# Performance work log

Measured on AMD Instinct MI355X. Metric: run time of the kernel, lower is better.

Reference implementation:

```python
import jax, jax.numpy as jnp
import numpy as np

B, T = 64, 256
IN, HID, OUT = 512, 1024, 256
NUM_DOMAINS = 20

def setup_inputs() -> dict:
    key = jax.random.key(0)
    k1, k2, k3, k4 = jax.random.split(key, 4)
    x = jax.random.normal(k1, (B, T, IN), dtype=jnp.float32)
    hetero_info = jax.random.randint(k2, (B, 2), 0, NUM_DOMAINS, dtype=jnp.int64)
    # embedding tables init N(0, 0.02) as in the torch module
    fc1_table = 0.02 * jax.random.normal(k3, (NUM_DOMAINS, IN * HID + HID), dtype=jnp.float32)
    fc2_table = 0.02 * jax.random.normal(k4, (NUM_DOMAINS, HID * OUT + OUT), dtype=jnp.float32)
    return {"x": x, "hetero_info": hetero_info, "fc1_table": fc1_table, "fc2_table": fc2_table}

def reference(x, hetero_info, fc1_table, fc2_table):
    domain_id = hetero_info[:, 0].astype(jnp.int32)
    Bn = domain_id.shape[0]
    fc1_param = fc1_table[domain_id]                     # (B, IN*HID + HID)
    w1 = fc1_param[:, : IN * HID].reshape(Bn, IN, HID)   # (B, IN, HID)
    b1 = fc1_param[:, IN * HID:].reshape(Bn, 1, HID)
    fc2_param = fc2_table[domain_id]                     # (B, HID*OUT + OUT)
    w2 = fc2_param[:, : HID * OUT].reshape(Bn, HID, OUT) # (B, HID, OUT)
    b2 = fc2_param[:, HID * OUT:].reshape(Bn, 1, OUT)
    h = jnp.einsum('bti,bih->bth', x, w1) + b1
    h = jax.nn.gelu(h, approximate=False)  # torch nn.GELU default = exact erf
    out = jnp.einsum('bth,bho->bto', h, w2) + b2
    return out
```

## Files before the change

kernel.cpp:

```cpp
#include <hip/hip_runtime.h>
#include <math.h>

#define B_  64
#define T_  256
#define IN_ 512
#define HID_ 1024
#define OUT_ 256
#define NDOM 20

typedef __bf16 bf16_t;
typedef __bf16 bf16x8 __attribute__((ext_vector_type(8)));
typedef __bf16 bf16x4 __attribute__((ext_vector_type(4)));
typedef float  f32x4  __attribute__((ext_vector_type(4)));

__device__ __forceinline__ unsigned f2bf_bits(float f) {
    unsigned u = __builtin_bit_cast(unsigned, f);
    return (u + 0x7FFFu + ((u >> 16) & 1u)) >> 16;
}
__device__ __forceinline__ unsigned pack_bf16x2(float x, float y) {
    return f2bf_bits(x) | (f2bf_bits(y) << 16);
}

__device__ __forceinline__ void gl_lds16(const void* g, void* l) {
    __builtin_amdgcn_global_load_lds(
        (const __attribute__((address_space(1))) unsigned*)g,
        (__attribute__((address_space(3))) unsigned*)l,
        16, 0, 0);
}

__device__ __forceinline__ float gelu_fast(float v) {
    const float t = v * 0.70710678118654752f;
    const float a = __builtin_fabsf(t);
    const float k = __builtin_amdgcn_rcpf(__builtin_fmaf(0.3275911f, a, 1.0f));
    float p = __builtin_fmaf(1.061405429f, k, -1.453152027f);
    p = __builtin_fmaf(p, k, 1.421413741f);
    p = __builtin_fmaf(p, k, -0.284496736f);
    p = __builtin_fmaf(p, k, 0.254829592f);
    p = p * k;
    const float e  = __expf(-a * a);
    const float er = __builtin_fmaf(-p, e, 1.0f);
    const float erf_t = __builtin_copysignf(er, t);
    return 0.5f * v * (1.0f + erf_t);
}

__global__ __launch_bounds__(256) void prep_all(
    const float* __restrict__ X,  bf16_t* __restrict__ Xbf,
    const float* __restrict__ T1, const float* __restrict__ T2,
    bf16_t* __restrict__ W1t, bf16_t* __restrict__ W2t,
    float* __restrict__ b1, float* __restrict__ b2)
{
    const int tid = threadIdx.x;
    int blk = blockIdx.x;

    if (blk < 2048) {
        #pragma unroll
        for (int r = 0; r < 4; ++r) {
            const size_t idx = (size_t)blk * 1024 + r * 256 + tid;
            float4 v = ((const float4*)X)[idx];
            uint2 p;
            p.x = pack_bf16x2(v.x, v.y);
            p.y = pack_bf16x2(v.z, v.w);
            ((uint2*)Xbf)[idx] = p;
        }
        return;
    }

    const float* table; bf16_t* Wt; float* Bias;
    int K, N, d, n0, k0;
    if (blk < 4608) {
        blk -= 2048;
        d = blk >> 7; const int rem = blk & 127;
        k0 = (rem >> 4) * 64; n0 = (rem & 15) * 64;
        K = 512; N = 1024; table = T1; Wt = W1t; Bias = b1;
    } else {
        blk -= 4608;
        d = blk >> 6; const int rem = blk & 63;
        k0 = (rem >> 2) * 64; n0 = (rem & 3) * 64;
        K = 1024; N = 256; table = T2; Wt = W2t; Bias = b2;
    }
    const float* W = table + (size_t)d * ((size_t)K * N + N);

    __shared__ float t[64][65];

    #pragma unroll
    for (int r = 0; r < 4; ++r) {
        const int kl = (tid >> 4) + r * 16;
        const int nl = (tid & 15) * 4;
        float4 v = *(const float4*)(W + (size_t)(k0 + kl) * N + n0 + nl);
        t[kl][nl + 0] = v.x; t[kl][nl + 1] = v.y;
        t[kl][nl + 2] = v.z; t[kl][nl + 3] = v.w;
    }
    __syncthreads();

    bf16_t* Wtd = Wt + (size_t)d * K * N;
    #pragma unroll
    for (int r = 0; r < 4; ++r) {
        const int nl = (tid >> 4) + r * 16;
        const int k4 = (tid & 15) * 4;
        uint2 p;
        p.x = pack_bf16x2(t[k4 + 0][nl], t[k4 + 1][nl]);
        p.y = pack_bf16x2(t[k4 + 2][nl], t[k4 + 3][nl]);
        *(uint2*)(Wtd + (size_t)(n0 + nl) * K + k0 + k4) = p;
    }

    if (k0 == 0 && tid < 64)
        Bias[(size_t)d * N + n0 + tid] = W[(size_t)K * N + n0 + tid];
}

#define CT_STRIDE 136
__global__ __launch_bounds__(256) void fc1_gemm(
    const bf16_t* __restrict__ Xbf,
    const bf16_t* __restrict__ W1t,
    const float*  __restrict__ Bias,
    const int*    __restrict__ hetero,
    bf16_t*       __restrict__ H)
{
    const int id   = blockIdx.x;
    const int g    = id & 127;
    const int nidx = id >> 7;
    const int b    = g >> 1;
    const int m0   = (g & 1) * 128;
    const int n0   = nidx * 128;
    const int d    = hetero[2 * b];
    const bf16_t* W    = W1t + (size_t)d * HID_ * IN_;
    const float*  bias = Bias + (size_t)d * HID_;
    const bf16_t* A    = Xbf + (size_t)(b * 256 + m0) * IN_;

    __shared__ __attribute__((aligned(16))) char smem[34816];

    const int tid  = threadIdx.x;
    const int wave = tid >> 6;
    const int lane = tid & 63;
    const int l16  = lane & 15;
    const int quad = lane >> 4;
    const int wm   = (wave >> 1) * 64;
    const int wn   = (wave & 1) * 64;

    f32x4 acc[4][4] = {};

    auto ldsA = [&](int nb) -> bf16_t* { return (bf16_t*)(smem + nb * 16384); };
    auto ldsB = [&](int nb) -> bf16_t* { return (bf16_t*)(smem + 8192 + nb * 16384); };

    auto stageA = [&](int kk, bf16_t* dst) {
        #pragma unroll
        for (int cc = 0; cc < 2; ++cc) {
            const int r0  = wave * 32 + cc * 16;
            const int row = r0 + (lane >> 2);
            const int cs  = (lane & 3) ^ ((row >> 1) & 3);
            gl_lds16(A + (size_t)row * IN_ + kk + cs * 8, dst + r0 * 32);
        }
    };
    auto stageB = [&](int kk, bf16_t* dst) {
        #pragma unroll
        for (int cc = 0; cc < 2; ++cc) {
            const int r0  = wave * 32 + cc * 16;
            const int row = r0 + (lane >> 2);
            const int cs  = (lane & 3) ^ ((row >> 1) & 3);
            gl_lds16(W + (size_t)(n0 + row) * IN_ + kk + cs * 8, dst + r0 * 32);
        }
    };
    auto compute = [&](const bf16_t* La, const bf16_t* Lb) {
        bf16x8 af[4], bfg[4];
        #pragma unroll
        for (int i = 0; i < 4; ++i) {
            const int r = wm + i * 16 + l16;
            const int c = quad ^ ((r >> 1) & 3);
            af[i] = *(const bf16x8*)&La[r * 32 + c * 8];
        }
        #pragma unroll
        for (int j = 0; j < 4; ++j) {
            const int r = wn + j * 16 + l16;
            const int c = quad ^ ((r >> 1) & 3);
            bfg[j] = *(const bf16x8*)&Lb[r * 32 + c * 8];
        }
        #pragma unroll
        for (int i = 0; i < 4; ++i)
            #pragma unroll
            for (int j = 0; j < 4; ++j)
                acc[i][j] = __builtin_amdgcn_mfma_f32_16x16x32_bf16(bfg[j], af[i], acc[i][j], 0, 0, 0);
    };

    stageA(0, ldsA(0));
    stageB(0, ldsB(0));
    __syncthreads();

    int buf = 0;
    for (int s = 0; s < 15; ++s) {
        stageA((s + 1) * 32, ldsA(buf ^ 1));
        stageB((s + 1) * 32, ldsB(buf ^ 1));
        compute(ldsA(buf), ldsB(buf));
        __syncthreads();
        buf ^= 1;
    }
    compute(ldsA(buf), ldsB(buf));
    __syncthreads();

    bf16_t* Ct = (bf16_t*)smem;

    #pragma unroll
    for (int i = 0; i < 4; ++i) {
        const int m = wm + i * 16 + l16;
        #pragma unroll
        for (int j = 0; j < 4; ++j) {
            const int nl = wn + j * 16 + quad * 4;
            const float4 b4 = *(const float4*)&bias[n0 + nl];
            bf16x4 w;
            w[0] = (bf16_t)gelu_fast(acc[i][j][0] + b4.x);
            w[1] = (bf16_t)gelu_fast(acc[i][j][1] + b4.y);
            w[2] = (bf16_t)gelu_fast(acc[i][j][2] + b4.z);
            w[3] = (bf16_t)gelu_fast(acc[i][j][3] + b4.w);
            *(bf16x4*)&Ct[m * CT_STRIDE + nl] = w;
        }
    }
    __syncthreads();

    #pragma unroll
    for (int it = 0; it < 8; ++it) {
        const int row = it * 16 + (tid >> 4);
        const int ch  = tid & 15;
        uint4 v = *(const uint4*)&Ct[row * CT_STRIDE + ch * 8];
        *(uint4*)&H[((size_t)(b * 256 + m0 + row)) * HID_ + n0 + ch * 8] = v;
    }
}

__global__ __launch_bounds__(256) void fc2_gemm(
    const bf16_t* __restrict__ H,
    const bf16_t* __restrict__ W2t,
    const float*  __restrict__ Bias,
    const int*    __restrict__ hetero,
    float*        __restrict__ Out)
{
    const int id   = blockIdx.x;
    const int g    = id & 255;
    const int nidx = id >> 8;
    const int b    = g >> 2;
    const int m0   = (g & 3) * 64;
    const int n0   = nidx * 128;
    const int d    = hetero[2 * b];
    const bf16_t* W    = W2t + (size_t)d * OUT_ * HID_;
    const float*  bias = Bias + (size_t)d * OUT_;
    const bf16_t* A    = H + (size_t)(b * 256 + m0) * HID_;

    __shared__ __attribute__((aligned(16))) char smem[49152];

    const int tid  = threadIdx.x;
    const int wave = tid >> 6;
    const int lane = tid & 63;
    const int l16  = lane & 15;
    const int quad = lane >> 4;
    const int wm   = (wave >> 1) * 32;
    const int wn   = (wave & 1) * 64;

    f32x4 acc[2][4] = {};

    auto ldsA = [&](int nb) -> bf16_t* { return (bf16_t*)(smem + nb * 24576); };
    auto ldsB = [&](int nb) -> bf16_t* { return (bf16_t*)(smem + 8192 + nb * 24576); };

    auto stage = [&](int kk, int nb) {
        bf16_t* dA = ldsA(nb);
        bf16_t* dB = ldsB(nb);
        #pragma unroll
        for (int cc = 0; cc < 2; ++cc) {
            const int r0  = wave * 16 + cc * 8;
            const int row = r0 + (lane >> 3);
            const int cs  = (lane & 7) ^ (row & 7);
            gl_lds16(A + (size_t)row * HID_ + kk + cs * 8, dA + r0 * 64);
        }
        #pragma unroll
        for (int cc = 0; cc < 4; ++cc) {
            const int r0  = wave * 32 + cc * 8;
            const int row = r0 + (lane >> 3);
            const int cs  = (lane & 7) ^ (row & 7);
            gl_lds16(W + (size_t)(n0 + row) * HID_ + kk + cs * 8, dB + r0 * 64);
        }
    };
    auto compute = [&](int nb) {
        const bf16_t* La = ldsA(nb);
        const bf16_t* Lb = ldsB(nb);
        #pragma unroll
        for (int h = 0; h < 2; ++h) {
            bf16x8 af[2], bfg[4];
            #pragma unroll
            for (int i = 0; i < 2; ++i) {
                const int r = wm + i * 16 + l16;
                const int c = (h * 4 + quad) ^ (r & 7);
                af[i] = *(const bf16x8*)&La[r * 64 + c * 8];
            }
            #pragma unroll
            for (int j = 0; j < 4; ++j) {
                const int r = wn + j * 16 + l16;
                const int c = (h * 4 + quad) ^ (r & 7);
                bfg[j] = *(const bf16x8*)&Lb[r * 64 + c * 8];
            }
            #pragma unroll
            for (int i = 0; i < 2; ++i)
                #pragma unroll
                for (int j = 0; j < 4; ++j)
                    acc[i][j] = __builtin_amdgcn_mfma_f32_16x16x32_bf16(bfg[j], af[i], acc[i][j], 0, 0, 0);
        }
    };

    stage(0, 0);
    __syncthreads();
    int buf = 0;
    for (int s = 0; s < 15; ++s) {
        stage((s + 1) * 64, buf ^ 1);
        compute(buf);
        __syncthreads();
        buf ^= 1;
    }
    compute(buf);

    #pragma unroll
    for (int i = 0; i < 2; ++i) {
        const int m = m0 + wm + i * 16 + l16;
        #pragma unroll
        for (int j = 0; j < 4; ++j) {
            const int nl = wn + j * 16 + quad * 4;
            const float4 b4 = *(const float4*)&bias[n0 + nl];
            float4 o;
            o.x = acc[i][j][0] + b4.x;
            o.y = acc[i][j][1] + b4.y;
            o.z = acc[i][j][2] + b4.z;
            o.w = acc[i][j][3] + b4.w;
            *(float4*)&Out[(size_t)(b * 256 + m) * OUT_ + n0 + nl] = o;
        }
    }
}

extern "C" void kernel_launch(void* const* d_in, const int* in_sizes, int n_in,
                              void* d_out, int out_size, void* d_ws, size_t ws_size,
                              hipStream_t stream) {
    const float* x         = (const float*)d_in[0];
    const int*   hetero    = (const int*)d_in[1];
    const float* fc1_table = (const float*)d_in[2];
    const float* fc2_table = (const float*)d_in[3];
    float*       out       = (float*)d_out;

    char* ws = (char*)d_ws;
    bf16_t* W1t = (bf16_t*)(ws);
    bf16_t* W2t = (bf16_t*)(ws + 20971520);
    float*  b1  = (float*)(ws + 31457280);
    float*  b2  = (float*)(ws + 31539200);
    bf16_t* H   = (bf16_t*)(ws + 31559680);

    bf16_t* Xbf = (bf16_t*)d_out;

    prep_all<<<dim3(5888), 256, 0, stream>>>(x, Xbf, fc1_table, fc2_table,
                                             W1t, W2t, b1, b2);
    fc1_gemm<<<dim3(1024), 256, 0, stream>>>(Xbf, W1t, b1, hetero, H);
    fc2_gemm<<<dim3(512), 256, 0, stream>>>(H, W2t, b2, hetero, out);
}
```

Before: 179.2 us.

## Triple-buffer LDS staging with partial vmcnt waits in both GEMMs

Both GEMM kernels move from a double-buffered LDS pipeline with full __syncthreads to a three-stage ring buffer. Two tiles are prefetched ahead, and an explicit s_waitcnt vmcnt(N) waits only for the older tile's global-to-LDS loads before a raw s_barrier. The goal is to keep more loads in flight and hide global memory latency behind MFMA compute. It raises LDS use (48KB and 72KB per block), which may cut occupancy, and correctness depends on the hand-counted vmcnt values matching the number of loads issued per stage.

```diff
diff --git a/kernel.cpp b/kernel.cpp
--- a/kernel.cpp
+++ b/kernel.cpp
@@ -27,6 +27,8 @@
         (__attribute__((address_space(3))) unsigned*)l,
         16, 0, 0);
 }
+
+#define WAITVM(N) asm volatile("s_waitcnt vmcnt(" #N ")" ::: "memory")
 
 __device__ __forceinline__ float gelu_fast(float v) {
     const float t = v * 0.70710678118654752f;
@@ -126,7 +128,7 @@
     const float*  bias = Bias + (size_t)d * HID_;
     const bf16_t* A    = Xbf + (size_t)(b * 256 + m0) * IN_;
 
-    __shared__ __attribute__((aligned(16))) char smem[34816];
+    __shared__ __attribute__((aligned(16))) char smem[49152];
 
     const int tid  = threadIdx.x;
     const int wave = tid >> 6;
@@ -180,19 +182,26 @@
                 acc[i][j] = __builtin_amdgcn_mfma_f32_16x16x32_bf16(bfg[j], af[i], acc[i][j], 0, 0, 0);
     };
 
-    stageA(0, ldsA(0));
-    stageB(0, ldsB(0));
-    __syncthreads();
-
-    int buf = 0;
-    for (int s = 0; s < 15; ++s) {
-        stageA((s + 1) * 32, ldsA(buf ^ 1));
-        stageB((s + 1) * 32, ldsB(buf ^ 1));
-        compute(ldsA(buf), ldsB(buf));
-        __syncthreads();
-        buf ^= 1;
-    }
-    compute(ldsA(buf), ldsB(buf));
+    stageA(0, ldsA(0));  stageB(0, ldsB(0));
+    stageA(32, ldsA(1)); stageB(32, ldsB(1));
+    WAITVM(4);
+    __builtin_amdgcn_s_barrier();
+
+    int cs_ = 2, cc_ = 0;
+    for (int s = 0; s < 14; ++s) {
+        stageA((s + 2) * 32, ldsA(cs_));
+        stageB((s + 2) * 32, ldsB(cs_));
+        compute(ldsA(cc_), ldsB(cc_));
+        WAITVM(4);
+        __builtin_amdgcn_s_barrier();
+        cs_ = (cs_ == 2) ? 0 : cs_ + 1;
+        cc_ = (cc_ == 2) ? 0 : cc_ + 1;
+    }
+    WAITVM(0);
+    __builtin_amdgcn_s_barrier();
+    compute(ldsA(cc_), ldsB(cc_));
+    cc_ = (cc_ == 2) ? 0 : cc_ + 1;
+    compute(ldsA(cc_), ldsB(cc_));
     __syncthreads();
 
     bf16_t* Ct = (bf16_t*)smem;
@@ -241,7 +250,7 @@
     const float*  bias = Bias + (size_t)d * OUT_;
     const bf16_t* A    = H + (size_t)(b * 256 + m0) * HID_;
 
-    __shared__ __attribute__((aligned(16))) char smem[49152];
+    __shared__ __attribute__((aligned(16))) char smem[73728];
 
     const int tid  = threadIdx.x;
     const int wave = tid >> 6;
@@ -301,15 +310,24 @@
     };
 
     stage(0, 0);
-    __syncthreads();
-    int buf = 0;
-    for (int s = 0; s < 15; ++s) {
-        stage((s + 1) * 64, buf ^ 1);
-        compute(buf);
-        __syncthreads();
-        buf ^= 1;
-    }
-    compute(buf);
+    stage(64, 1);
+    WAITVM(6);
+    __builtin_amdgcn_s_barrier();
+
+    int cs_ = 2, cc_ = 0;
+    for (int s = 0; s < 14; ++s) {
+        stage((s + 2) * 64, cs_);
+        compute(cc_);
+        WAITVM(6);
+        __builtin_amdgcn_s_barrier();
+        cs_ = (cs_ == 2) ? 0 : cs_ + 1;
+        cc_ = (cc_ == 2) ? 0 : cc_ + 1;
+    }
+    WAITVM(0);
+    __builtin_amdgcn_s_barrier();
+    compute(cc_);
+    cc_ = (cc_ == 2) ? 0 : cc_ + 1;
+    compute(cc_);
 
     #pragma unroll
     for (int i = 0; i < 2; ++i) {
```

Result: no change. 181.5 us (+1.3%).
